# Kernel optimization log

Hardware: AMD Instinct MI355X
Metric: run time of the kernel (lower is better)

The kernel has to match this reference:

```python
import jax, jax.numpy as jnp
import numpy as np

EPS = 1e-6
SLIDING_WINDOW = 512
SCALING = 256.0 ** -0.5  # query_pre_attn_scalar ** -0.5


def rmsnorm(x, w):
    rms = jnp.sqrt(jnp.mean(jnp.square(x), axis=-1, keepdims=True) + EPS)
    return (x / rms) * (1.0 + w)


def apply_rope(x, cos, sin):
    # x: [B,S,H,D]; cos/sin: [S,D//2] -> pairs of adjacent dims rotated as complex
    B, S, H, D = x.shape
    xr = x.reshape(B, S, H, D // 2, 2)
    a, b = xr[..., 0], xr[..., 1]
    c = cos[None, :, None, :]
    s = sin[None, :, None, :]
    out = jnp.stack([a * c - b * s, a * s + b * c], axis=-1)
    return out.reshape(B, S, H, D)


def setup_inputs() -> dict:
    key = jax.random.key(0)
    ks = jax.random.split(key, 8)
    B, S, E, H, D = 2, 4096, 640, 4, 256
    x = jax.random.normal(ks[0], (B, S, E), dtype=jnp.float32)
    # RoPE tables (rope_local_base=10000 for sliding layers)
    inv_freq = 1.0 / (10000.0 ** (np.arange(0, D, 2, dtype=np.float32) / D))
    t = np.arange(S, dtype=np.float32)
    freqs = np.outer(t, inv_freq)  # [S, D//2]
    cos = jnp.asarray(np.cos(freqs), dtype=jnp.float32)
    sin = jnp.asarray(np.sin(freqs), dtype=jnp.float32)
    sc = 1.0 / np.sqrt(E)
    Wq = jax.random.normal(ks[1], (E, H * D), dtype=jnp.float32) * sc
    Wk = jax.random.normal(ks[2], (E, 1 * D), dtype=jnp.float32) * sc
    Wv = jax.random.normal(ks[3], (E, 1 * D), dtype=jnp.float32) * sc
    Wo = jax.random.normal(ks[4], (H * D, E), dtype=jnp.float32) * (1.0 / np.sqrt(H * D))
    q_norm_w = jnp.zeros((D,), dtype=jnp.float32)  # torch init: zeros, acts as weight 1+0
    k_norm_w = jnp.zeros((D,), dtype=jnp.float32)
    return {"x": x, "cos": cos, "sin": sin, "Wq": Wq, "Wk": Wk, "Wv": Wv,
            "Wo": Wo, "q_norm_w": q_norm_w, "k_norm_w": k_norm_w}


def reference(x, cos, sin, Wq, Wk, Wv, Wo, q_norm_w, k_norm_w):
    B, S, E = x.shape
    H, D = 4, 256
    q = (x @ Wq).reshape(B, S, H, D)
    k = (x @ Wk).reshape(B, S, 1, D)
    v = (x @ Wv).reshape(B, S, 1, D)
    q = rmsnorm(q, q_norm_w)
    k = rmsnorm(k, k_norm_w)
    q = apply_rope(q, cos, sin)
    k = apply_rope(k, cos, sin)
    k0 = k[:, :, 0, :]  # [B,S,D] single KV head (MQA)
    v0 = v[:, :, 0, :]
    scores = jnp.einsum('bqhd,bkd->bhqk', q, k0) * SCALING  # [B,H,S,S]
    i = jnp.arange(S)[:, None]
    j = jnp.arange(S)[None, :]
    # causal AND within sliding window: 0 <= i-j <= W
    allowed = (j <= i) & (i - j <= SLIDING_WINDOW)
    scores = jnp.where(allowed[None, None], scores, -jnp.inf)
    attn = jax.nn.softmax(scores, axis=-1)
    out = jnp.einsum('bhqk,bkd->bqhd', attn, v0).reshape(B, S, H * D)
    return out @ Wo
```

## Files before the change

### kernel.cpp

```cpp
#include <hip/hip_runtime.h>
#include <hip/hip_bf16.h>

#define S_LEN 4096
#define NH 4
#define HD 256
#define WIN 512
#define ATT_SCALE 0.0625f
#define QKV_N 1536

typedef short s16x8 __attribute__((ext_vector_type(8)));
typedef float f32x4 __attribute__((ext_vector_type(4)));

static __device__ inline unsigned short f2bf(float f) {
  union { float f; unsigned int u; } v; v.f = f;
  unsigned int r = v.u + 0x7fff + ((v.u >> 16) & 1);
  return (unsigned short)(r >> 16);
}
static __device__ inline float bf2f(unsigned short h) {
  union { unsigned int u; float f; } v; v.u = ((unsigned int)h) << 16;
  return v.f;
}
static __device__ inline void gl2lds16(const void* g, void* l) {
  __builtin_amdgcn_global_load_lds(
      (const __attribute__((address_space(1))) unsigned int*)g,
      (__attribute__((address_space(3))) unsigned int*)l, 16, 0, 0);
}

__global__ __launch_bounds__(256) void cvt_bf16_kernel(const float* __restrict__ src,
                                                       unsigned short* __restrict__ dst,
                                                       int n4) {
  const int t = blockIdx.x * 256 + threadIdx.x;
  if (t >= n4) return;
  const float4 v = ((const float4*)src)[t];
  const unsigned int p0 = f2bf(v.x) | ((unsigned int)f2bf(v.y) << 16);
  const unsigned int p1 = f2bf(v.z) | ((unsigned int)f2bf(v.w) << 16);
  *(uint2*)(dst + (size_t)t * 4) = make_uint2(p0, p1);
}

__global__ __launch_bounds__(256) void trcast64_kernel(const float* __restrict__ src,
                                                       unsigned short* __restrict__ dst,
                                                       int K, int N) {
  __shared__ float ts[64][65];
  const int bn = blockIdx.x, bk = blockIdx.y;
  const int tid = threadIdx.x;
#pragma unroll
  for (int it = 0; it < 4; ++it) {
    const int c = it * 256 + tid;
    const int row = c >> 4, col4 = (c & 15) << 2;
    const float4 v = *(const float4*)(src + (size_t)(bk * 64 + row) * N + bn * 64 + col4);
    ts[row][col4 + 0] = v.x; ts[row][col4 + 1] = v.y;
    ts[row][col4 + 2] = v.z; ts[row][col4 + 3] = v.w;
  }
  __syncthreads();
#pragma unroll
  for (int it = 0; it < 4; ++it) {
    const int c = it * 256 + tid;
    const int nrow = c >> 4, kc4 = (c & 15) << 2;
    const unsigned int p0 = f2bf(ts[kc4 + 0][nrow]) | ((unsigned int)f2bf(ts[kc4 + 1][nrow]) << 16);
    const unsigned int p1 = f2bf(ts[kc4 + 2][nrow]) | ((unsigned int)f2bf(ts[kc4 + 3][nrow]) << 16);
    *(uint2*)(dst + (size_t)(bn * 64 + nrow) * K + bk * 64 + kc4) = make_uint2(p0, p1);
  }
}

template <bool BF16OUT>
__global__ __launch_bounds__(256) void gemm_bt(const unsigned short* __restrict__ A,
                                               const unsigned short* __restrict__ Bt,
                                               void* __restrict__ Cv,
                                               int M, int N, int K) {
  __shared__ unsigned short As[128 * 32];
  __shared__ unsigned short Bs[128 * 32];
  const int tid = threadIdx.x;
  const int wave = tid >> 6, lane = tid & 63;
  const int ln15 = lane & 15, lgr = lane >> 4;
  const int bm = blockIdx.y, bn = blockIdx.x;
  const int wr = wave & 1, wc = wave >> 1;
  const unsigned short* Ab = A + (size_t)bm * 128 * K;
  const unsigned short* Bb = Bt + (size_t)bn * 128 * K;

  f32x4 acc[4][4];
#pragma unroll
  for (int mt = 0; mt < 4; ++mt)
#pragma unroll
    for (int nt = 0; nt < 4; ++nt) acc[mt][nt] = (f32x4){0.f, 0.f, 0.f, 0.f};

  for (int kt = 0; kt < K; kt += 32) {
#pragma unroll
    for (int i = 0; i < 2; ++i) {
      const int c = tid + 256 * i;
      const int row = c >> 2, kc = (c & 3) << 3;
      gl2lds16(Ab + (size_t)row * K + kt + kc, &As[c * 8]);
      gl2lds16(Bb + (size_t)row * K + kt + kc, &Bs[c * 8]);
    }
    __syncthreads();
    s16x8 af[4], bfr[4];
#pragma unroll
    for (int t = 0; t < 4; ++t) {
      af[t]  = *(const s16x8*)&As[(wr * 64 + t * 16 + ln15) * 32 + lgr * 8];
      bfr[t] = *(const s16x8*)&Bs[(wc * 64 + t * 16 + ln15) * 32 + lgr * 8];
    }
#pragma unroll
    for (int mt = 0; mt < 4; ++mt)
#pragma unroll
      for (int nt = 0; nt < 4; ++nt)
        acc[mt][nt] = __builtin_amdgcn_mfma_f32_16x16x32_bf16(af[mt], bfr[nt], acc[mt][nt], 0, 0, 0);
    __syncthreads();
  }

#pragma unroll
  for (int mt = 0; mt < 4; ++mt)
#pragma unroll
    for (int nt = 0; nt < 4; ++nt)
#pragma unroll
      for (int r = 0; r < 4; ++r) {
        const size_t row = bm * 128 + wr * 64 + mt * 16 + lgr * 4 + r;
        const size_t col = bn * 128 + wc * 64 + nt * 16 + ln15;
        if (BF16OUT) ((unsigned short*)Cv)[row * N + col] = f2bf(acc[mt][nt][r]);
        else         ((float*)Cv)[row * N + col] = acc[mt][nt][r];
      }
}

__global__ __launch_bounds__(256) void normrope_kernel(
    unsigned short* __restrict__ qkv,
    const float* __restrict__ cosb, const float* __restrict__ sinb,
    const float* __restrict__ qw, const float* __restrict__ kw) {
  const int idx = blockIdx.x;
  const int h = idx % 5;
  const int bs = idx / 5;
  const int s = bs & (S_LEN - 1);
  unsigned short* base = qkv + (size_t)bs * QKV_N;
  unsigned short* row; const float* w; float oscale;
  if (h < 4) { row = base + h * HD;  w = qw; oscale = ATT_SCALE; }
  else       { row = base + 4 * HD;  w = kw; oscale = 1.0f; }
  const int tid = threadIdx.x;
  const int lane = tid & 63, wave = tid >> 6;
  __shared__ float xs[HD];
  __shared__ float red[4];
  const float xv = bf2f(row[tid]);
  xs[tid] = xv;
  float ssq = xv * xv;
#pragma unroll
  for (int off = 32; off > 0; off >>= 1) ssq += __shfl_xor(ssq, off);
  if (lane == 0) red[wave] = ssq;
  __syncthreads();
  const float tot = red[0] + red[1] + red[2] + red[3];
  const float inv = rsqrtf(tot * (1.0f / 256.0f) + 1e-6f);
  const int pi = tid >> 1;
  const float c = cosb[s * (HD / 2) + pi];
  const float sn = sinb[s * (HD / 2) + pi];
  const float a = xs[pi * 2]     * inv * (1.0f + w[pi * 2]);
  const float b = xs[pi * 2 + 1] * inv * (1.0f + w[pi * 2 + 1]);
  const float outv = ((tid & 1) ? (a * sn + b * c) : (a * c - b * sn)) * oscale;
  row[tid] = f2bf(outv);
}

__global__ __launch_bounds__(256) void vtranspose_kernel(
    const unsigned short* __restrict__ qkv, unsigned short* __restrict__ vtb) {
  __shared__ unsigned short ts[32][264];
  const int b = blockIdx.x >> 7, jt = blockIdx.x & 127;
  const int tid = threadIdx.x;
  const unsigned short* src = qkv + ((size_t)(b * S_LEN) + jt * 32) * QKV_N + 5 * HD;
#pragma unroll
  for (int it = 0; it < 4; ++it) {
    const int c = tid + 256 * it;
    const int row = c >> 5, col8 = (c & 31) << 3;
    *(uint4*)&ts[row][col8] = *(const uint4*)(src + (size_t)row * QKV_N + col8);
  }
  __syncthreads();
  unsigned short tmp[32];
#pragma unroll
  for (int jj = 0; jj < 32; ++jj) tmp[jj] = ts[jj][tid];
  unsigned short* dst = vtb + ((size_t)(b * 128 + jt) * 256 + tid) * 32;
#pragma unroll
  for (int wq = 0; wq < 4; ++wq) *(uint4*)(dst + wq * 8) = *(uint4*)(tmp + wq * 8);
}

#define PS_LD 40

__global__ __launch_bounds__(256) void attn_mfma_kernel(
    const unsigned short* __restrict__ qkv, const unsigned short* __restrict__ vtb,
    unsigned short* __restrict__ aob) {
  const int g = blockIdx.x;
  const int xcd = g & 7, slot = g >> 3;
  const int h = slot >> 4;
  const int qt = xcd * 16 + (slot & 15);
  const int b = qt >> 6;
  const int q0 = (qt & 63) << 6;
  const int tid = threadIdx.x;
  const int wave = tid >> 6;
  const int lane = tid & 63;
  const int ln15 = lane & 15;
  const int lgr = lane >> 4;

  __shared__ unsigned short Ks[2][16 * 512];
  __shared__ unsigned short Vts[2][16 * 512];
  __shared__ unsigned short Ps[4][16 * PS_LD];

  const size_t qrow = (size_t)(b * S_LEN + q0 + wave * 16 + ln15) * QKV_N + h * HD;
  s16x8 qfrag[8];
#pragma unroll
  for (int f = 0; f < 8; ++f)
    qfrag[f] = *(const s16x8*)(qkv + qrow + f * 32 + lgr * 8);

  f32x4 acc[16];
#pragma unroll
  for (int t = 0; t < 16; ++t) acc[t] = (f32x4){0.f, 0.f, 0.f, 0.f};
  float l_part[4] = {0.f, 0.f, 0.f, 0.f};

  const int kt_lo = max(0, q0 - WIN) >> 5;
  const int kt_hi = (q0 + 63) >> 5;
  const unsigned short* kbase = qkv + (size_t)(b * S_LEN) * QKV_N + 4 * HD;
  const unsigned short* vbase = vtb + (size_t)b * (S_LEN / 32) * HD * 32;

  auto stage = [&](int kt, int buf) {
#pragma unroll
    for (int u = 0; u < 4; ++u) {
      const int c = wave * 4 + u;
      const int ct = c >> 3, f = c & 7;
      const unsigned short* gk =
          kbase + (size_t)(kt * 32 + ct * 16 + ln15) * QKV_N + f * 32 + lgr * 8;
      gl2lds16(gk, &Ks[buf][c * 512]);
      const unsigned short* gv =
          vbase + (size_t)kt * (HD * 32) + (size_t)(c * 16 + ln15) * 32 + lgr * 8;
      gl2lds16(gv, &Vts[buf][c * 512]);
    }
  };

  stage(kt_lo, 0);
  __syncthreads();

  unsigned short* psw = Ps[wave];
  const int i_row0 = q0 + wave * 16 + lgr * 4;

  for (int kt = kt_lo; kt <= kt_hi; ++kt) {
    const int cur = (kt - kt_lo) & 1;
    if (kt < kt_hi) stage(kt + 1, cur ^ 1);

    f32x4 sc[2];
    sc[0] = (f32x4){0.f, 0.f, 0.f, 0.f};
    sc[1] = (f32x4){0.f, 0.f, 0.f, 0.f};
#pragma unroll
    for (int f = 0; f < 8; ++f) {
#pragma unroll
      for (int ct = 0; ct < 2; ++ct) {
        const s16x8 kf = *(const s16x8*)&Ks[cur][(ct * 8 + f) * 512 + lane * 8];
        sc[ct] = __builtin_amdgcn_mfma_f32_16x16x32_bf16(qfrag[f], kf, sc[ct], 0, 0, 0);
      }
    }

    const int j0 = kt * 32 + ln15;
    float p0[4], p1[4];
#pragma unroll
    for (int r = 0; r < 4; ++r) {
      const int i = i_row0 + r;
      const bool a0 = (j0 <= i) && (i - j0 <= WIN);
      const bool a1 = (j0 + 16 <= i) && (i - (j0 + 16) <= WIN);
      const float e0 = __expf(sc[0][r] - 16.0f);
      const float e1 = __expf(sc[1][r] - 16.0f);
      p0[r] = a0 ? e0 : 0.0f;
      p1[r] = a1 ? e1 : 0.0f;
      l_part[r] += p0[r] + p1[r];
    }
#pragma unroll
    for (int r = 0; r < 4; ++r) {
      psw[(lgr * 4 + r) * PS_LD + ln15]      = f2bf(p0[r]);
      psw[(lgr * 4 + r) * PS_LD + 16 + ln15] = f2bf(p1[r]);
    }
    const s16x8 pf = *(const s16x8*)&psw[ln15 * PS_LD + lgr * 8];
#pragma unroll
    for (int t = 0; t < 16; ++t) {
      const s16x8 vf = *(const s16x8*)&Vts[cur][t * 512 + lane * 8];
      acc[t] = __builtin_amdgcn_mfma_f32_16x16x32_bf16(pf, vf, acc[t], 0, 0, 0);
    }
    __syncthreads();
  }

#pragma unroll
  for (int off = 1; off < 16; off <<= 1)
#pragma unroll
    for (int r = 0; r < 4; ++r) l_part[r] += __shfl_xor(l_part[r], off);

  float inv_l[4];
#pragma unroll
  for (int r = 0; r < 4; ++r) inv_l[r] = 1.0f / l_part[r];
#pragma unroll
  for (int t = 0; t < 16; ++t)
#pragma unroll
    for (int r = 0; r < 4; ++r) {
      const size_t orow = (size_t)(b * S_LEN + q0 + wave * 16 + lgr * 4 + r);
      aob[(orow * NH + h) * HD + t * 16 + ln15] = f2bf(acc[t][r] * inv_l[r]);
    }
}

extern "C" void kernel_launch(void* const* d_in, const int* in_sizes, int n_in,
                              void* d_out, int out_size, void* d_ws, size_t ws_size,
                              hipStream_t stream) {
  const float* x    = (const float*)d_in[0];
  const float* cosb = (const float*)d_in[1];
  const float* sinb = (const float*)d_in[2];
  const float* Wq   = (const float*)d_in[3];
  const float* Wk   = (const float*)d_in[4];
  const float* Wv   = (const float*)d_in[5];
  const float* Wo   = (const float*)d_in[6];
  const float* qw   = (const float*)d_in[7];
  const float* kw   = (const float*)d_in[8];
  float* out = (float*)d_out;

  unsigned short* ws = (unsigned short*)d_ws;
  unsigned short* xb     = ws;
  unsigned short* Wqkvt  = xb + 5242880;
  unsigned short* Wot    = Wqkvt + 983040;
  unsigned short* qkvb   = Wot + 655360;
  unsigned short* vtb    = qkvb + 12582912;
  unsigned short* aob    = vtb + 2097152;
  const int M = 2 * S_LEN;

  cvt_bf16_kernel<<<(M * 640 / 4 + 255) / 256, 256, 0, stream>>>(x, xb, M * 640 / 4);
  trcast64_kernel<<<dim3(1024 / 64, 640 / 64), 256, 0, stream>>>(Wq, Wqkvt, 640, 1024);
  trcast64_kernel<<<dim3(256 / 64, 640 / 64), 256, 0, stream>>>(Wk, Wqkvt + (size_t)1024 * 640, 640, 256);
  trcast64_kernel<<<dim3(256 / 64, 640 / 64), 256, 0, stream>>>(Wv, Wqkvt + (size_t)1280 * 640, 640, 256);
  trcast64_kernel<<<dim3(640 / 64, 1024 / 64), 256, 0, stream>>>(Wo, Wot, 1024, 640);
  gemm_bt<true><<<dim3(QKV_N / 128, M / 128), 256, 0, stream>>>(xb, Wqkvt, qkvb, M, QKV_N, 640);
  normrope_kernel<<<M * 5, 256, 0, stream>>>(qkvb, cosb, sinb, qw, kw);
  vtranspose_kernel<<<256, 256, 0, stream>>>(qkvb, vtb);
  attn_mfma_kernel<<<M / 64 * NH, 256, 0, stream>>>(qkvb, vtb, aob);
  gemm_bt<false><<<dim3(640 / 128, M / 128), 256, 0, stream>>>(aob, Wot, out, M, 640, 1024);
}
```

Measured before the change: 231.2 us.

## Fuse prep and normrope/transpose launches, use 64-row tiles for output GEMM

Merges the x cast and four weight transpose-casts into one prep kernel, and merges the norm/RoPE kernel with the V transpose into a single launch, cutting per-launch overhead. Replaces the output projection GEMM with a 64x128-tile variant so more blocks cover the small 640-wide output. Also packs two bf16 probability stores into one 32-bit LDS write in attention and reorders the V transpose reads. The fused kernels carry extra branching and shared-memory footprint, and the smaller tile reduces operand reuse.

```diff
diff --git a/kernel.cpp b/kernel.cpp
--- a/kernel.cpp
+++ b/kernel.cpp
@@ -26,39 +26,55 @@
       (__attribute__((address_space(3))) unsigned int*)l, 16, 0, 0);
 }
 
-__global__ __launch_bounds__(256) void cvt_bf16_kernel(const float* __restrict__ src,
-                                                       unsigned short* __restrict__ dst,
-                                                       int n4) {
-  const int t = blockIdx.x * 256 + threadIdx.x;
-  if (t >= n4) return;
-  const float4 v = ((const float4*)src)[t];
-  const unsigned int p0 = f2bf(v.x) | ((unsigned int)f2bf(v.y) << 16);
-  const unsigned int p1 = f2bf(v.z) | ((unsigned int)f2bf(v.w) << 16);
-  *(uint2*)(dst + (size_t)t * 4) = make_uint2(p0, p1);
-}
-
-__global__ __launch_bounds__(256) void trcast64_kernel(const float* __restrict__ src,
-                                                       unsigned short* __restrict__ dst,
-                                                       int K, int N) {
-  __shared__ float ts[64][65];
-  const int bn = blockIdx.x, bk = blockIdx.y;
-  const int tid = threadIdx.x;
+static __device__ void trcast_tile(const float* __restrict__ src,
+                                   unsigned short* __restrict__ dst,
+                                   int K, int N, int bn, int bk, int tid,
+                                   float* ts ) {
 #pragma unroll
   for (int it = 0; it < 4; ++it) {
     const int c = it * 256 + tid;
     const int row = c >> 4, col4 = (c & 15) << 2;
     const float4 v = *(const float4*)(src + (size_t)(bk * 64 + row) * N + bn * 64 + col4);
-    ts[row][col4 + 0] = v.x; ts[row][col4 + 1] = v.y;
-    ts[row][col4 + 2] = v.z; ts[row][col4 + 3] = v.w;
+    ts[row * 65 + col4 + 0] = v.x; ts[row * 65 + col4 + 1] = v.y;
+    ts[row * 65 + col4 + 2] = v.z; ts[row * 65 + col4 + 3] = v.w;
   }
   __syncthreads();
 #pragma unroll
   for (int it = 0; it < 4; ++it) {
     const int c = it * 256 + tid;
     const int nrow = c >> 4, kc4 = (c & 15) << 2;
-    const unsigned int p0 = f2bf(ts[kc4 + 0][nrow]) | ((unsigned int)f2bf(ts[kc4 + 1][nrow]) << 16);
-    const unsigned int p1 = f2bf(ts[kc4 + 2][nrow]) | ((unsigned int)f2bf(ts[kc4 + 3][nrow]) << 16);
+    const unsigned int p0 = f2bf(ts[(kc4 + 0) * 65 + nrow]) | ((unsigned int)f2bf(ts[(kc4 + 1) * 65 + nrow]) << 16);
+    const unsigned int p1 = f2bf(ts[(kc4 + 2) * 65 + nrow]) | ((unsigned int)f2bf(ts[(kc4 + 3) * 65 + nrow]) << 16);
     *(uint2*)(dst + (size_t)(bn * 64 + nrow) * K + bk * 64 + kc4) = make_uint2(p0, p1);
+  }
+}
+
+__global__ __launch_bounds__(256) void prep_kernel(
+    const float* __restrict__ x, unsigned short* __restrict__ xb,
+    const float* __restrict__ Wq, const float* __restrict__ Wk,
+    const float* __restrict__ Wv, const float* __restrict__ Wo,
+    unsigned short* __restrict__ Wqkvt, unsigned short* __restrict__ Wot) {
+  __shared__ float ts[64 * 65];
+  const int g = blockIdx.x;
+  const int tid = threadIdx.x;
+  if (g < 5120) {
+    const int t = g * 256 + tid;
+    const float4 v = ((const float4*)x)[t];
+    const unsigned int p0 = f2bf(v.x) | ((unsigned int)f2bf(v.y) << 16);
+    const unsigned int p1 = f2bf(v.z) | ((unsigned int)f2bf(v.w) << 16);
+    *(uint2*)(xb + (size_t)t * 4) = make_uint2(p0, p1);
+  } else if (g < 5280) {
+    const int g2 = g - 5120;
+    trcast_tile(Wq, Wqkvt, 640, 1024, g2 & 15, g2 >> 4, tid, ts);
+  } else if (g < 5320) {
+    const int g2 = g - 5280;
+    trcast_tile(Wk, Wqkvt + (size_t)1024 * 640, 640, 256, g2 & 3, g2 >> 2, tid, ts);
+  } else if (g < 5360) {
+    const int g2 = g - 5320;
+    trcast_tile(Wv, Wqkvt + (size_t)1280 * 640, 640, 256, g2 & 3, g2 >> 2, tid, ts);
+  } else {
+    const int g2 = g - 5360;
+    trcast_tile(Wo, Wot, 1024, 640, g2 % 10, g2 / 10, tid, ts);
   }
 }
 
@@ -119,59 +135,120 @@
       }
 }
 
-__global__ __launch_bounds__(256) void normrope_kernel(
+__global__ __launch_bounds__(256) void gemm_bt64(const unsigned short* __restrict__ A,
+                                                 const unsigned short* __restrict__ Bt,
+                                                 float* __restrict__ C,
+                                                 int M, int N, int K) {
+  __shared__ unsigned short As[64 * 32];
+  __shared__ unsigned short Bs[128 * 32];
+  const int tid = threadIdx.x;
+  const int wave = tid >> 6, lane = tid & 63;
+  const int ln15 = lane & 15, lgr = lane >> 4;
+  const int bm = blockIdx.y, bn = blockIdx.x;
+  const unsigned short* Ab = A + (size_t)bm * 64 * K;
+  const unsigned short* Bb = Bt + (size_t)bn * 128 * K;
+
+  f32x4 acc[4][2];
+#pragma unroll
+  for (int mt = 0; mt < 4; ++mt)
+#pragma unroll
+    for (int nt = 0; nt < 2; ++nt) acc[mt][nt] = (f32x4){0.f, 0.f, 0.f, 0.f};
+
+  for (int kt = 0; kt < K; kt += 32) {
+    {
+      const int row = tid >> 2, kc = (tid & 3) << 3;
+      gl2lds16(Ab + (size_t)row * K + kt + kc, &As[tid * 8]);
+#pragma unroll
+      for (int i = 0; i < 2; ++i) {
+        const int c = tid + 256 * i;
+        const int brow = c >> 2, bkc = (c & 3) << 3;
+        gl2lds16(Bb + (size_t)brow * K + kt + bkc, &Bs[c * 8]);
+      }
+    }
+    __syncthreads();
+    s16x8 af[4], bfr[2];
+#pragma unroll
+    for (int t = 0; t < 4; ++t)
+      af[t] = *(const s16x8*)&As[(t * 16 + ln15) * 32 + lgr * 8];
+#pragma unroll
+    for (int t = 0; t < 2; ++t)
+      bfr[t] = *(const s16x8*)&Bs[(wave * 32 + t * 16 + ln15) * 32 + lgr * 8];
+#pragma unroll
+    for (int mt = 0; mt < 4; ++mt)
+#pragma unroll
+      for (int nt = 0; nt < 2; ++nt)
+        acc[mt][nt] = __builtin_amdgcn_mfma_f32_16x16x32_bf16(af[mt], bfr[nt], acc[mt][nt], 0, 0, 0);
+    __syncthreads();
+  }
+
+#pragma unroll
+  for (int mt = 0; mt < 4; ++mt)
+#pragma unroll
+    for (int nt = 0; nt < 2; ++nt)
+#pragma unroll
+      for (int r = 0; r < 4; ++r) {
+        const size_t row = bm * 64 + mt * 16 + lgr * 4 + r;
+        const size_t col = bn * 128 + wave * 32 + nt * 16 + ln15;
+        C[row * N + col] = acc[mt][nt][r];
+      }
+}
+
+__global__ __launch_bounds__(256) void normrope_vt_kernel(
     unsigned short* __restrict__ qkv,
     const float* __restrict__ cosb, const float* __restrict__ sinb,
-    const float* __restrict__ qw, const float* __restrict__ kw) {
+    const float* __restrict__ qw, const float* __restrict__ kw,
+    unsigned short* __restrict__ vtb) {
   const int idx = blockIdx.x;
-  const int h = idx % 5;
-  const int bs = idx / 5;
-  const int s = bs & (S_LEN - 1);
-  unsigned short* base = qkv + (size_t)bs * QKV_N;
-  unsigned short* row; const float* w; float oscale;
-  if (h < 4) { row = base + h * HD;  w = qw; oscale = ATT_SCALE; }
-  else       { row = base + 4 * HD;  w = kw; oscale = 1.0f; }
-  const int tid = threadIdx.x;
-  const int lane = tid & 63, wave = tid >> 6;
-  __shared__ float xs[HD];
-  __shared__ float red[4];
-  const float xv = bf2f(row[tid]);
-  xs[tid] = xv;
-  float ssq = xv * xv;
-#pragma unroll
-  for (int off = 32; off > 0; off >>= 1) ssq += __shfl_xor(ssq, off);
-  if (lane == 0) red[wave] = ssq;
-  __syncthreads();
-  const float tot = red[0] + red[1] + red[2] + red[3];
-  const float inv = rsqrtf(tot * (1.0f / 256.0f) + 1e-6f);
-  const int pi = tid >> 1;
-  const float c = cosb[s * (HD / 2) + pi];
-  const float sn = sinb[s * (HD / 2) + pi];
-  const float a = xs[pi * 2]     * inv * (1.0f + w[pi * 2]);
-  const float b = xs[pi * 2 + 1] * inv * (1.0f + w[pi * 2 + 1]);
-  const float outv = ((tid & 1) ? (a * sn + b * c) : (a * c - b * sn)) * oscale;
-  row[tid] = f2bf(outv);
-}
-
-__global__ __launch_bounds__(256) void vtranspose_kernel(
-    const unsigned short* __restrict__ qkv, unsigned short* __restrict__ vtb) {
-  __shared__ unsigned short ts[32][264];
-  const int b = blockIdx.x >> 7, jt = blockIdx.x & 127;
-  const int tid = threadIdx.x;
-  const unsigned short* src = qkv + ((size_t)(b * S_LEN) + jt * 32) * QKV_N + 5 * HD;
-#pragma unroll
-  for (int it = 0; it < 4; ++it) {
-    const int c = tid + 256 * it;
-    const int row = c >> 5, col8 = (c & 31) << 3;
-    *(uint4*)&ts[row][col8] = *(const uint4*)(src + (size_t)row * QKV_N + col8);
-  }
-  __syncthreads();
-  unsigned short tmp[32];
-#pragma unroll
-  for (int jj = 0; jj < 32; ++jj) tmp[jj] = ts[jj][tid];
-  unsigned short* dst = vtb + ((size_t)(b * 128 + jt) * 256 + tid) * 32;
-#pragma unroll
-  for (int wq = 0; wq < 4; ++wq) *(uint4*)(dst + wq * 8) = *(uint4*)(tmp + wq * 8);
+  const int tid = threadIdx.x;
+  if (idx < 40960) {
+    const int h = idx % 5;
+    const int bs = idx / 5;
+    const int s = bs & (S_LEN - 1);
+    unsigned short* base = qkv + (size_t)bs * QKV_N;
+    unsigned short* row; const float* w; float oscale;
+    if (h < 4) { row = base + h * HD;  w = qw; oscale = ATT_SCALE; }
+    else       { row = base + 4 * HD;  w = kw; oscale = 1.0f; }
+    const int lane = tid & 63, wave = tid >> 6;
+    __shared__ float xs[HD];
+    __shared__ float red[4];
+    const float xv = bf2f(row[tid]);
+    xs[tid] = xv;
+    float ssq = xv * xv;
+#pragma unroll
+    for (int off = 32; off > 0; off >>= 1) ssq += __shfl_xor(ssq, off);
+    if (lane == 0) red[wave] = ssq;
+    __syncthreads();
+    const float tot = red[0] + red[1] + red[2] + red[3];
+    const float inv = rsqrtf(tot * (1.0f / 256.0f) + 1e-6f);
+    const int pi = tid >> 1;
+    const float c = cosb[s * (HD / 2) + pi];
+    const float sn = sinb[s * (HD / 2) + pi];
+    const float a = xs[pi * 2]     * inv * (1.0f + w[pi * 2]);
+    const float b = xs[pi * 2 + 1] * inv * (1.0f + w[pi * 2 + 1]);
+    const float outv = ((tid & 1) ? (a * sn + b * c) : (a * c - b * sn)) * oscale;
+    row[tid] = f2bf(outv);
+  } else {
+    __shared__ unsigned short ts[32][264];
+    const int g2 = idx - 40960;
+    const int b = g2 >> 7, jt = g2 & 127;
+    const unsigned short* src = qkv + ((size_t)(b * S_LEN) + jt * 32) * QKV_N + 5 * HD;
+#pragma unroll
+    for (int it = 0; it < 4; ++it) {
+      const int c = tid + 256 * it;
+      const int row = c >> 5, col8 = (c & 31) << 3;
+      *(uint4*)&ts[row][col8] = *(const uint4*)(src + (size_t)row * QKV_N + col8);
+    }
+    __syncthreads();
+    unsigned short tmp[32];
+#pragma unroll
+    for (int s2 = 0; s2 < 32; ++s2) {
+      const int jj = (s2 >> 1) | ((s2 & 1) << 4);
+      tmp[s2] = ts[jj][tid];
+    }
+    unsigned short* dst = vtb + ((size_t)(b * 128 + jt) * 256 + tid) * 32;
+#pragma unroll
+    for (int wq = 0; wq < 4; ++wq) *(uint4*)(dst + wq * 8) = *(uint4*)(tmp + wq * 8);
+  }
 }
 
 #define PS_LD 40
@@ -262,8 +339,8 @@
     }
 #pragma unroll
     for (int r = 0; r < 4; ++r) {
-      psw[(lgr * 4 + r) * PS_LD + ln15]      = f2bf(p0[r]);
-      psw[(lgr * 4 + r) * PS_LD + 16 + ln15] = f2bf(p1[r]);
+      const unsigned int pk = (unsigned int)f2bf(p0[r]) | ((unsigned int)f2bf(p1[r]) << 16);
+      *(unsigned int*)&psw[(lgr * 4 + r) * PS_LD + (ln15 << 1)] = pk;
     }
     const s16x8 pf = *(const s16x8*)&psw[ln15 * PS_LD + lgr * 8];
 #pragma unroll
@@ -314,14 +391,9 @@
   unsigned short* aob    = vtb + 2097152;
   const int M = 2 * S_LEN;
 
-  cvt_bf16_kernel<<<(M * 640 / 4 + 255) / 256, 256, 0, stream>>>(x, xb, M * 640 / 4);
-  trcast64_kernel<<<dim3(1024 / 64, 640 / 64), 256, 0, stream>>>(Wq, Wqkvt, 640, 1024);
-  trcast64_kernel<<<dim3(256 / 64, 640 / 64), 256, 0, stream>>>(Wk, Wqkvt + (size_t)1024 * 640, 640, 256);
-  trcast64_kernel<<<dim3(256 / 64, 640 / 64), 256, 0, stream>>>(Wv, Wqkvt + (size_t)1280 * 640, 640, 256);
-  trcast64_kernel<<<dim3(640 / 64, 1024 / 64), 256, 0, stream>>>(Wo, Wot, 1024, 640);
+  prep_kernel<<<5520, 256, 0, stream>>>(x, xb, Wq, Wk, Wv, Wo, Wqkvt, Wot);
   gemm_bt<true><<<dim3(QKV_N / 128, M / 128), 256, 0, stream>>>(xb, Wqkvt, qkvb, M, QKV_N, 640);
-  normrope_kernel<<<M * 5, 256, 0, stream>>>(qkvb, cosb, sinb, qw, kw);
-  vtranspose_kernel<<<256, 256, 0, stream>>>(qkvb, vtb);
+  normrope_vt_kernel<<<M * 5 + 256, 256, 0, stream>>>(qkvb, cosb, sinb, qw, kw, vtb);
   attn_mfma_kernel<<<M / 64 * NH, 256, 0, stream>>>(qkvb, vtb, aob);
-  gemm_bt<false><<<dim3(640 / 128, M / 128), 256, 0, stream>>>(aob, Wot, out, M, 640, 1024);
-}
+  gemm_bt64<<<dim3(640 / 128, M / 64), 256, 0, stream>>>(aob, Wot, out, M, 640, 1024);
+}
```

After: 215.4 us. 1.07x faster.
